# Optimization experiments

Measured on AMD Instinct MI355X. Metric: run time of the kernel, lower is better.

The kernel has to match this reference:

```python
import jax, jax.numpy as jnp
import numpy as np

N, E = 50000, 640000
D_IN, D_HID, D_OUT, HEADS = 128, 128, 128, 2


def _lin_init(k, fan_in, fan_out):
    return jax.random.normal(k, (fan_in, fan_out), jnp.float32) / np.sqrt(fan_in)


def setup_inputs() -> dict:
    key = jax.random.key(0)
    ks = jax.random.split(key, 20)
    inp = {
        "x": jax.random.normal(ks[0], (N, D_IN), jnp.float32),
        "edge_index": jax.random.randint(ks[1], (2, E), 0, N, dtype=jnp.int32),
    }
    # layer 1: in -> hid (heads*per_head = 2 * 64 = 128)
    inp["Wq1"] = _lin_init(ks[2], D_IN, D_HID); inp["bq1"] = jnp.zeros((D_HID,), jnp.float32)
    inp["Wk1"] = _lin_init(ks[3], D_IN, D_HID); inp["bk1"] = jnp.zeros((D_HID,), jnp.float32)
    inp["Wv1"] = _lin_init(ks[4], D_IN, D_HID); inp["bv1"] = jnp.zeros((D_HID,), jnp.float32)
    inp["Ws1"] = _lin_init(ks[5], D_IN, D_HID); inp["bs1"] = jnp.zeros((D_HID,), jnp.float32)
    # layer 2: hid -> out
    inp["Wq2"] = _lin_init(ks[6], D_HID, D_OUT); inp["bq2"] = jnp.zeros((D_OUT,), jnp.float32)
    inp["Wk2"] = _lin_init(ks[7], D_HID, D_OUT); inp["bk2"] = jnp.zeros((D_OUT,), jnp.float32)
    inp["Wv2"] = _lin_init(ks[8], D_HID, D_OUT); inp["bv2"] = jnp.zeros((D_OUT,), jnp.float32)
    inp["Ws2"] = _lin_init(ks[9], D_HID, D_OUT); inp["bs2"] = jnp.zeros((D_OUT,), jnp.float32)
    return inp


def _transformer_conv(x, src, dst, Wq, bq, Wk, bk, Wv, bv, Ws, bs, heads):
    """PyG TransformerConv (concat=True, root_weight=True, eval mode)."""
    n = x.shape[0]
    C = Wq.shape[1] // heads  # per-head channels
    q = (x @ Wq + bq).reshape(n, heads, C)
    k = (x @ Wk + bk).reshape(n, heads, C)
    v = (x @ Wv + bv).reshape(n, heads, C)
    qi = q[dst]              # [E, H, C] gather at destination
    kj = k[src]              # [E, H, C] gather at source
    vj = v[src]              # [E, H, C]
    alpha = jnp.sum(qi * kj, axis=-1) / np.sqrt(C)   # [E, H]
    # segment softmax over incoming edges of each destination node
    amax = jax.ops.segment_max(alpha, dst, num_segments=n)   # [N, H]
    ex = jnp.exp(alpha - amax[dst])                            # [E, H]
    denom = jax.ops.segment_sum(ex, dst, num_segments=n)      # [N, H]
    a = ex / denom[dst]                                        # [E, H]
    msg = vj * a[..., None]                                    # [E, H, C]
    out = jax.ops.segment_sum(msg, dst, num_segments=n).reshape(n, heads * C)
    return out + x @ Ws + bs  # root (skip) connection


def reference(x, edge_index, Wq1, bq1, Wk1, bk1, Wv1, bv1, Ws1, bs1,
              Wq2, bq2, Wk2, bk2, Wv2, bv2, Ws2, bs2):
    src, dst = edge_index[0], edge_index[1]
    h = _transformer_conv(x, src, dst, Wq1, bq1, Wk1, bk1, Wv1, bv1, Ws1, bs1, HEADS)
    h = jax.nn.relu(h)
    return _transformer_conv(h, src, dst, Wq2, bq2, Wk2, bk2, Wv2, bv2, Ws2, bs2, HEADS)
```

## Files before the change

kernel.cpp:

```cpp
#include <hip/hip_runtime.h>
#include <math.h>

#define D 128

typedef float  f32x4  __attribute__((ext_vector_type(4)));
typedef short  bf16x8 __attribute__((ext_vector_type(8)));

__device__ inline unsigned short bf16r(float f) {
    unsigned u = __float_as_uint(f);
    u = (u + 0x7fff + ((u >> 16) & 1)) >> 16;
    return (unsigned short)u;
}
__device__ inline unsigned bf16pair(float a, float b) {
    return (unsigned)bf16r(a) | ((unsigned)bf16r(b) << 16);
}
__device__ inline float bf16lo(unsigned w) { return __uint_as_float(w << 16); }
__device__ inline float bf16hi(unsigned w) { return __uint_as_float(w & 0xffff0000u); }

__device__ inline void unpack8(uint4 w, float* f) {
    f[0] = bf16lo(w.x); f[1] = bf16hi(w.x);
    f[2] = bf16lo(w.y); f[3] = bf16hi(w.y);
    f[4] = bf16lo(w.z); f[5] = bf16hi(w.z);
    f[6] = bf16lo(w.w); f[7] = bf16hi(w.w);
}

__global__ __launch_bounds__(256)
void prep(const float* __restrict__ X, unsigned* __restrict__ Xb, int npairs,
          const float* __restrict__ W0, const float* __restrict__ W1,
          const float* __restrict__ W2, const float* __restrict__ W3,
          const float* __restrict__ W4, const float* __restrict__ W5,
          const float* __restrict__ W6, const float* __restrict__ W7,
          unsigned short* __restrict__ Wt,
          int* __restrict__ cnt, int* __restrict__ bh, int* __restrict__ bcur, int n)
{
    const int nxb = (npairs + 255) >> 8;
    const int nz  = (n + 255) >> 8;
    const int b = blockIdx.x;
    if (b < nxb) {
        int i = b * 256 + threadIdx.x;
        if (i < npairs) {
            float2 v = *(const float2*)&X[2 * i];
            Xb[i] = bf16pair(v.x, v.y);
        }
    } else if (b < nxb + nz) {
        int i = (b - nxb) * 256 + threadIdx.x;
        if (i < n) cnt[i] = 0;
    } else if (b < nxb + nz + 8) {
        int wi = b - nxb - nz;
        const float* Ws[8] = {W0, W1, W2, W3, W4, W5, W6, W7};
        const float* W = Ws[wi];
        unsigned short* o = Wt + wi * 16384;
        for (int i = threadIdx.x; i < 16384; i += 256) {
            int k = i >> 7, c = i & 127;
            o[c * 128 + k] = bf16r(W[i]);
        }
    } else {
        if (threadIdx.x < 64) { bh[threadIdx.x] = 0; bcur[threadIdx.x] = 0; }
    }
}

__global__ __launch_bounds__(256)
void gemm_mfma(const unsigned short* __restrict__ Xb, int n,
               const unsigned short* __restrict__ Wtall,
               const float* __restrict__ bq, const float* __restrict__ bk,
               const float* __restrict__ bv, const float* __restrict__ bs,
               unsigned short* __restrict__ Qp, unsigned short* __restrict__ Kp,
               unsigned short* __restrict__ Vp, unsigned short* __restrict__ Sp)
{
    const int w = blockIdx.x;
    const int rowBase = blockIdx.y * 128;
    const unsigned short* W = Wtall + w * 16384;
    const float* bias = (w == 0) ? bq : (w == 1) ? bk : (w == 2) ? bv : bs;
    unsigned short* plane = (w == 0) ? Qp : (w == 1) ? Kp : (w == 2) ? Vp : Sp;

    __shared__ unsigned short Asm[128 * 136];

    const int tid  = threadIdx.x;
    const int wave = tid >> 6;
    const int lane = tid & 63;
    const int wr   = wave >> 1;
    const int wc   = wave & 1;
    const int q16  = lane >> 4;
    const int r16  = lane & 15;

    #pragma unroll
    for (int i = 0; i < 8; ++i) {
        int g = tid + 256 * i;
        int m = g >> 4, c = g & 15;
        int row = rowBase + m; if (row >= n) row = n - 1;
        uint4 da = *(const uint4*)(Xb + (size_t)row * 128 + c * 8);
        *(uint4*)&Asm[m * 136 + c * 8] = da;
    }

    const unsigned short* Wbase = W + (size_t)(wc * 64 + r16) * 128 + q16 * 8;
    bf16x8 bcur[4], bnxt[4];
    #pragma unroll
    for (int nj = 0; nj < 4; ++nj)
        bcur[nj] = *(const bf16x8*)(Wbase + nj * 16 * 128);

    __syncthreads();

    f32x4 acc[4][4];
    #pragma unroll
    for (int mi = 0; mi < 4; ++mi)
        #pragma unroll
        for (int nj = 0; nj < 4; ++nj) acc[mi][nj] = (f32x4)(0.f);

    #pragma unroll
    for (int kc = 0; kc < 4; ++kc) {
        if (kc < 3) {
            #pragma unroll
            for (int nj = 0; nj < 4; ++nj)
                bnxt[nj] = *(const bf16x8*)(Wbase + nj * 16 * 128 + (kc + 1) * 32);
        }
        bf16x8 a[4];
        #pragma unroll
        for (int mi = 0; mi < 4; ++mi)
            a[mi] = *(const bf16x8*)&Asm[(wr * 64 + mi * 16 + r16) * 136 + kc * 32 + q16 * 8];
        #pragma unroll
        for (int mi = 0; mi < 4; ++mi)
            #pragma unroll
            for (int nj = 0; nj < 4; ++nj)
                acc[mi][nj] = __builtin_amdgcn_mfma_f32_16x16x32_bf16(a[mi], bcur[nj], acc[mi][nj], 0, 0, 0);
        #pragma unroll
        for (int nj = 0; nj < 4; ++nj) bcur[nj] = bnxt[nj];
    }

    __syncthreads();
    #pragma unroll
    for (int nj = 0; nj < 4; ++nj) {
        const int col = wc * 64 + nj * 16 + r16;
        const float bias_c = bias[col];
        #pragma unroll
        for (int mi = 0; mi < 4; ++mi) {
            const int rbase = wr * 64 + mi * 16 + q16 * 4;
            #pragma unroll
            for (int r = 0; r < 4; ++r)
                Asm[(rbase + r) * 132 + col] = bf16r(acc[mi][nj][r] + bias_c);
        }
    }
    __syncthreads();
    #pragma unroll
    for (int i = 0; i < 8; ++i) {
        int g = tid + 256 * i;
        int m = g >> 4, c = g & 15;
        int row = rowBase + m;
        if (row < n) {
            uint4 d2 = *(const uint4*)&Asm[m * 132 + c * 8];
            *(uint4*)(plane + (size_t)row * 128 + c * 8) = d2;
        }
    }
}

__global__ void degree_hist(const int* __restrict__ dst, int e,
                            int* __restrict__ cnt, int* __restrict__ rank)
{
    int i = blockIdx.x * blockDim.x + threadIdx.x;
    if (i < e) rank[i] = atomicAdd(&cnt[dst[i]], 1);
}

__global__ __launch_bounds__(256)
void scan_hist(const int* __restrict__ cnt, int n, int* __restrict__ bsum, int* __restrict__ bh)
{
    __shared__ int sm[256];
    __shared__ int lh[64];
    if (threadIdx.x < 64) lh[threadIdx.x] = 0;
    int i = blockIdx.x * 256 + threadIdx.x;
    int v = (i < n) ? cnt[i] : 0;
    sm[threadIdx.x] = v;
    __syncthreads();
    if (i < n) atomicAdd(&lh[min(v, 63)], 1);
    #pragma unroll
    for (int off = 128; off > 0; off >>= 1) {
        if (threadIdx.x < off) sm[threadIdx.x] += sm[threadIdx.x + off];
        __syncthreads();
    }
    if (threadIdx.x == 0) bsum[blockIdx.x] = sm[0];
    if (threadIdx.x < 64 && lh[threadIdx.x] > 0)
        atomicAdd(&bh[threadIdx.x], lh[threadIdx.x]);
}

__global__ __launch_bounds__(256)
void scan2(int* __restrict__ bsum, int nb, const int* __restrict__ bh, int* __restrict__ boff)
{
    __shared__ int sm[256];
    int v = (threadIdx.x < nb) ? bsum[threadIdx.x] : 0;
    sm[threadIdx.x] = v;
    __syncthreads();
    int acc = v;
    for (int off = 1; off < 256; off <<= 1) {
        int t = (threadIdx.x >= off) ? sm[threadIdx.x - off] : 0;
        __syncthreads();
        acc += t;
        sm[threadIdx.x] = acc;
        __syncthreads();
    }
    if (threadIdx.x < nb) bsum[threadIdx.x] = acc - v;
    if (threadIdx.x == 0) {
        int run = 0;
        for (int b = 63; b >= 0; --b) { boff[b] = run; run += bh[b]; }
    }
}

__global__ __launch_bounds__(256)
void scan3_scatter(const int* __restrict__ cnt, const int* __restrict__ bsum,
                   int* __restrict__ row_ptr, int n, int e,
                   const int* __restrict__ boff, int* __restrict__ bcur,
                   int* __restrict__ perm)
{
    __shared__ int sm[256];
    __shared__ int lh[64];
    __shared__ int lbase[64];
    if (threadIdx.x < 64) lh[threadIdx.x] = 0;
    __syncthreads();
    int i = blockIdx.x * 256 + threadIdx.x;
    int v = (i < n) ? cnt[i] : 0;
    sm[threadIdx.x] = v;
    int b = 0, local = 0;
    if (i < n) {
        b = min(v, 63);
        local = atomicAdd(&lh[b], 1);
    }
    __syncthreads();
    int acc = v;
    for (int off = 1; off < 256; off <<= 1) {
        int t = (threadIdx.x >= off) ? sm[threadIdx.x - off] : 0;
        __syncthreads();
        acc += t;
        sm[threadIdx.x] = acc;
        __syncthreads();
    }
    if (i < n) row_ptr[i] = bsum[blockIdx.x] + acc - v;
    if (blockIdx.x == 0 && threadIdx.x == 0) row_ptr[n] = e;
    if (threadIdx.x < 64 && lh[threadIdx.x] > 0)
        lbase[threadIdx.x] = atomicAdd(&bcur[threadIdx.x], lh[threadIdx.x]);
    __syncthreads();
    if (i < n) perm[boff[b] + lbase[b] + local] = i;
}

__global__ void edge_scatter(const int* __restrict__ src, const int* __restrict__ dst, int e,
                             const int* __restrict__ row_ptr, const int* __restrict__ rank,
                             int* __restrict__ csr_src)
{
    int i = blockIdx.x * blockDim.x + threadIdx.x;
    if (i < e) {
        int d = dst[i];
        csr_src[row_ptr[d] + rank[i]] = src[i];
    }
}

__global__ __launch_bounds__(256)
void attn(const uint4* __restrict__ Qp, const uint4* __restrict__ Kp,
          const uint4* __restrict__ Vp, const uint4* __restrict__ Sp,
          const int* __restrict__ row_ptr, const int* __restrict__ csr_src,
          const int* __restrict__ perm,
          float* __restrict__ outf, uint4* __restrict__ outb,
          int n, int do_relu)
{
    const int wid  = (blockIdx.x * 256 + threadIdx.x) >> 6;
    const int lane = threadIdx.x & 63;
    const int nq   = lane >> 4;
    const int l16  = lane & 15;
    const int nidx = wid * 4 + nq;
    const int node = (nidx < n) ? perm[nidx] : -1;

    float q[8];
    int beg = 0, end = 0;
    if (node >= 0) {
        uint4 qw = Qp[(size_t)node * 16 + l16];
        unpack8(qw, q);
        beg = row_ptr[node];
        end = row_ptr[node + 1];
    }

    float m = -INFINITY, l = 0.f;
    float acc[8] = {0.f, 0.f, 0.f, 0.f, 0.f, 0.f, 0.f, 0.f};

    int i = beg;
    while (i + 4 <= end) {
        int s0 = csr_src[i], s1 = csr_src[i+1], s2 = csr_src[i+2], s3 = csr_src[i+3];
        uint4 kw0 = Kp[(size_t)s0 * 16 + l16];
        uint4 kw1 = Kp[(size_t)s1 * 16 + l16];
        uint4 kw2 = Kp[(size_t)s2 * 16 + l16];
        uint4 kw3 = Kp[(size_t)s3 * 16 + l16];
        uint4 vw0 = Vp[(size_t)s0 * 16 + l16];
        uint4 vw1 = Vp[(size_t)s1 * 16 + l16];
        uint4 vw2 = Vp[(size_t)s2 * 16 + l16];
        uint4 vw3 = Vp[(size_t)s3 * 16 + l16];

        float kf[8];
        unpack8(kw0, kf);
        float d0 = q[0]*kf[0]+q[1]*kf[1]+q[2]*kf[2]+q[3]*kf[3]+q[4]*kf[4]+q[5]*kf[5]+q[6]*kf[6]+q[7]*kf[7];
        unpack8(kw1, kf);
        float d1 = q[0]*kf[0]+q[1]*kf[1]+q[2]*kf[2]+q[3]*kf[3]+q[4]*kf[4]+q[5]*kf[5]+q[6]*kf[6]+q[7]*kf[7];
        unpack8(kw2, kf);
        float d2 = q[0]*kf[0]+q[1]*kf[1]+q[2]*kf[2]+q[3]*kf[3]+q[4]*kf[4]+q[5]*kf[5]+q[6]*kf[6]+q[7]*kf[7];
        unpack8(kw3, kf);
        float d3 = q[0]*kf[0]+q[1]*kf[1]+q[2]*kf[2]+q[3]*kf[3]+q[4]*kf[4]+q[5]*kf[5]+q[6]*kf[6]+q[7]*kf[7];

        d0 += __shfl_xor(d0, 4, 64); d1 += __shfl_xor(d1, 4, 64);
        d2 += __shfl_xor(d2, 4, 64); d3 += __shfl_xor(d3, 4, 64);
        d0 += __shfl_xor(d0, 2, 64); d1 += __shfl_xor(d1, 2, 64);
        d2 += __shfl_xor(d2, 2, 64); d3 += __shfl_xor(d3, 2, 64);
        d0 += __shfl_xor(d0, 1, 64); d1 += __shfl_xor(d1, 1, 64);
        d2 += __shfl_xor(d2, 1, 64); d3 += __shfl_xor(d3, 1, 64);

        float a0 = d0 * 0.125f, a1 = d1 * 0.125f, a2 = d2 * 0.125f, a3 = d3 * 0.125f;
        float m4 = fmaxf(fmaxf(a0, a1), fmaxf(a2, a3));
        float mn = fmaxf(m, m4);
        float corr = __expf(m - mn);
        float p0 = __expf(a0 - mn), p1 = __expf(a1 - mn);
        float p2 = __expf(a2 - mn), p3 = __expf(a3 - mn);
        l = l * corr + (p0 + p1 + p2 + p3);

        float v0f[8], v1f[8], v2f[8], v3f[8];
        unpack8(vw0, v0f); unpack8(vw1, v1f); unpack8(vw2, v2f); unpack8(vw3, v3f);
        #pragma unroll
        for (int c2 = 0; c2 < 8; ++c2) {
            float t = acc[c2] * corr;
            t += p0 * v0f[c2]; t += p1 * v1f[c2];
            t += p2 * v2f[c2]; t += p3 * v3f[c2];
            acc[c2] = t;
        }
        m = mn;
        i += 4;
    }
    while (i < end) {
        int s = csr_src[i];
        uint4 kw = Kp[(size_t)s * 16 + l16];
        uint4 vw = Vp[(size_t)s * 16 + l16];
        float kf[8], vf[8];
        unpack8(kw, kf); unpack8(vw, vf);
        float part = q[0]*kf[0]+q[1]*kf[1]+q[2]*kf[2]+q[3]*kf[3]+q[4]*kf[4]+q[5]*kf[5]+q[6]*kf[6]+q[7]*kf[7];
        part += __shfl_xor(part, 4, 64);
        part += __shfl_xor(part, 2, 64);
        part += __shfl_xor(part, 1, 64);
        float alpha = part * 0.125f;
        float mn = fmaxf(m, alpha);
        float corr = __expf(m - mn);
        float p = __expf(alpha - mn);
        l = l * corr + p;
        #pragma unroll
        for (int c2 = 0; c2 < 8; ++c2) acc[c2] = acc[c2] * corr + p * vf[c2];
        m = mn;
        ++i;
    }

    if (node >= 0) {
        float inv = (l > 0.f) ? (1.f / l) : 0.f;
        float sv[8];
        unpack8(Sp[(size_t)node * 16 + l16], sv);
        float r[8];
        #pragma unroll
        for (int c2 = 0; c2 < 8; ++c2) r[c2] = acc[c2] * inv + sv[c2];
        if (do_relu) {
            #pragma unroll
            for (int c2 = 0; c2 < 8; ++c2) r[c2] = fmaxf(r[c2], 0.f);
        }
        if (outb) {
            uint4 o;
            o.x = bf16pair(r[0], r[1]); o.y = bf16pair(r[2], r[3]);
            o.z = bf16pair(r[4], r[5]); o.w = bf16pair(r[6], r[7]);
            outb[(size_t)node * 16 + l16] = o;
        } else {
            *(float4*)&outf[(size_t)node * 128 + l16 * 8]     = make_float4(r[0], r[1], r[2], r[3]);
            *(float4*)&outf[(size_t)node * 128 + l16 * 8 + 4] = make_float4(r[4], r[5], r[6], r[7]);
        }
    }
}

extern "C" void kernel_launch(void* const* d_in, const int* in_sizes, int n_in,
                              void* d_out, int out_size, void* d_ws, size_t ws_size,
                              hipStream_t stream)
{
    const float* x    = (const float*)d_in[0];
    const int*   edge = (const int*)d_in[1];
    const int n = in_sizes[0] / D;
    const int e = in_sizes[1] / 2;
    const int* srcv = edge;
    const int* dstv = edge + e;

    const float* Wq1 = (const float*)d_in[2];  const float* bq1 = (const float*)d_in[3];
    const float* Wk1 = (const float*)d_in[4];  const float* bk1 = (const float*)d_in[5];
    const float* Wv1 = (const float*)d_in[6];  const float* bv1 = (const float*)d_in[7];
    const float* Ws1 = (const float*)d_in[8];  const float* bs1 = (const float*)d_in[9];
    const float* Wq2 = (const float*)d_in[10]; const float* bq2 = (const float*)d_in[11];
    const float* Wk2 = (const float*)d_in[12]; const float* bk2 = (const float*)d_in[13];
    const float* Wv2 = (const float*)d_in[14]; const float* bv2 = (const float*)d_in[15];
    const float* Ws2 = (const float*)d_in[16]; const float* bs2 = (const float*)d_in[17];

    char* wsb = (char*)d_ws;
    size_t off = 0;
    auto alloc = [&](size_t bytes) -> void* {
        void* p = wsb + off;
        off += (bytes + 255) & ~(size_t)255;
        return p;
    };
    unsigned short* Qp = (unsigned short*)alloc((size_t)n * D * sizeof(unsigned short));
    unsigned short* Kp = (unsigned short*)alloc((size_t)n * D * sizeof(unsigned short));
    unsigned short* Vp = (unsigned short*)alloc((size_t)n * D * sizeof(unsigned short));
    unsigned short* Sp = (unsigned short*)alloc((size_t)n * D * sizeof(unsigned short));
    unsigned short* Xb = (unsigned short*)alloc((size_t)n * D * sizeof(unsigned short));
    unsigned short* Hu = (unsigned short*)alloc((size_t)n * D * sizeof(unsigned short));
    unsigned short* Wt = (unsigned short*)alloc(8 * 16384 * sizeof(unsigned short));
    int* cnt     = (int*)alloc((size_t)n * sizeof(int));
    int* row_ptr = (int*)alloc((size_t)(n + 1) * sizeof(int));
    int* bsum    = (int*)alloc(1024 * sizeof(int));
    int* perm    = (int*)alloc((size_t)n * sizeof(int));
    int* bh      = (int*)alloc(64 * sizeof(int));
    int* bcur    = (int*)alloc(64 * sizeof(int));
    int* boff    = (int*)alloc(64 * sizeof(int));
    int* rank    = (int*)alloc((size_t)e * sizeof(int));
    int* csr_src = (int*)alloc((size_t)e * sizeof(int));
    (void)ws_size; (void)n_in; (void)out_size;

    const int nb  = (n + 255) / 256;
    const int npairs = n * 64;
    const int nprep  = (npairs + 255) / 256 + nb + 8 + 1;

    prep<<<nprep, 256, 0, stream>>>(x, (unsigned*)Xb, npairs,
        Wq1, Wk1, Wv1, Ws1, Wq2, Wk2, Wv2, Ws2, Wt, cnt, bh, bcur, n);

    degree_hist<<<(e + 255) / 256, 256, 0, stream>>>(dstv, e, cnt, rank);
    scan_hist<<<nb, 256, 0, stream>>>(cnt, n, bsum, bh);
    scan2<<<1, 256, 0, stream>>>(bsum, nb, bh, boff);
    scan3_scatter<<<nb, 256, 0, stream>>>(cnt, bsum, row_ptr, n, e, boff, bcur, perm);
    edge_scatter<<<(e + 255) / 256, 256, 0, stream>>>(srcv, dstv, e, row_ptr, rank, csr_src);

    const dim3 ggrid(4, (n + 127) / 128);
    const int ablocks = ((n + 3) / 4 + 3) / 4;

    gemm_mfma<<<ggrid, 256, 0, stream>>>(Xb, n, Wt, bq1, bk1, bv1, bs1, Qp, Kp, Vp, Sp);
    attn<<<ablocks, 256, 0, stream>>>((const uint4*)Qp, (const uint4*)Kp, (const uint4*)Vp,
                                      (const uint4*)Sp, row_ptr, csr_src, perm,
                                      nullptr, (uint4*)Hu, n, 1);

    gemm_mfma<<<ggrid, 256, 0, stream>>>(Hu, n, Wt + 4 * 16384, bq2, bk2, bv2, bs2, Qp, Kp, Vp, Sp);
    attn<<<ablocks, 256, 0, stream>>>((const uint4*)Qp, (const uint4*)Kp, (const uint4*)Vp,
                                      (const uint4*)Sp, row_ptr, csr_src, perm,
                                      (float*)d_out, nullptr, n, 0);
}
```

Measured before the change: 338.0 us.

## Interleave K and V rows and software-pipeline edge gathers in attention

The GEMM now writes K and V into one interleaved buffer, 256 bf16 per node, so each source node's K and V sit in one contiguous 512-byte row. The attention kernel gathers from this combined buffer and double-buffers the 4-edge batches: it loads the next batch's K/V before computing on the current one, to hide gather latency. The double buffering needs more registers for the extra uint4 sets, which may lower occupancy.

```diff
diff --git a/kernel.cpp b/kernel.cpp
--- a/kernel.cpp
+++ b/kernel.cpp
@@ -64,14 +64,18 @@
                const unsigned short* __restrict__ Wtall,
                const float* __restrict__ bq, const float* __restrict__ bk,
                const float* __restrict__ bv, const float* __restrict__ bs,
-               unsigned short* __restrict__ Qp, unsigned short* __restrict__ Kp,
-               unsigned short* __restrict__ Vp, unsigned short* __restrict__ Sp)
+               unsigned short* __restrict__ Qp, unsigned short* __restrict__ KVp,
+               unsigned short* __restrict__ Sp)
 {
     const int w = blockIdx.x;
     const int rowBase = blockIdx.y * 128;
     const unsigned short* W = Wtall + w * 16384;
     const float* bias = (w == 0) ? bq : (w == 1) ? bk : (w == 2) ? bv : bs;
-    unsigned short* plane = (w == 0) ? Qp : (w == 1) ? Kp : (w == 2) ? Vp : Sp;
+    unsigned short* base; int rstride, coff;
+    if (w == 0)      { base = Qp;  rstride = 128; coff = 0; }
+    else if (w == 1) { base = KVp; rstride = 256; coff = 0; }
+    else if (w == 2) { base = KVp; rstride = 256; coff = 128; }
+    else             { base = Sp;  rstride = 128; coff = 0; }
 
     __shared__ unsigned short Asm[128 * 136];
 
@@ -147,7 +151,7 @@
         int row = rowBase + m;
         if (row < n) {
             uint4 d2 = *(const uint4*)&Asm[m * 132 + c * 8];
-            *(uint4*)(plane + (size_t)row * 128 + c * 8) = d2;
+            *(uint4*)(base + (size_t)row * rstride + coff + c * 8) = d2;
         }
     }
 }
@@ -249,9 +253,59 @@
     }
 }
 
-__global__ __launch_bounds__(256)
-void attn(const uint4* __restrict__ Qp, const uint4* __restrict__ Kp,
-          const uint4* __restrict__ Vp, const uint4* __restrict__ Sp,
+__device__ inline void load4(const uint4* __restrict__ KV, const int* __restrict__ csr,
+                             int i, int l16, uint4* k, uint4* v)
+{
+    int s0 = csr[i], s1 = csr[i+1], s2 = csr[i+2], s3 = csr[i+3];
+    k[0] = KV[(size_t)s0 * 32 + l16];      v[0] = KV[(size_t)s0 * 32 + 16 + l16];
+    k[1] = KV[(size_t)s1 * 32 + l16];      v[1] = KV[(size_t)s1 * 32 + 16 + l16];
+    k[2] = KV[(size_t)s2 * 32 + l16];      v[2] = KV[(size_t)s2 * 32 + 16 + l16];
+    k[3] = KV[(size_t)s3 * 32 + l16];      v[3] = KV[(size_t)s3 * 32 + 16 + l16];
+}
+
+__device__ inline void consume4(const uint4* k, const uint4* v, const float* q,
+                                float& m, float& l, float* acc)
+{
+    float kf[8];
+    unpack8(k[0], kf);
+    float d0 = q[0]*kf[0]+q[1]*kf[1]+q[2]*kf[2]+q[3]*kf[3]+q[4]*kf[4]+q[5]*kf[5]+q[6]*kf[6]+q[7]*kf[7];
+    unpack8(k[1], kf);
+    float d1 = q[0]*kf[0]+q[1]*kf[1]+q[2]*kf[2]+q[3]*kf[3]+q[4]*kf[4]+q[5]*kf[5]+q[6]*kf[6]+q[7]*kf[7];
+    unpack8(k[2], kf);
+    float d2 = q[0]*kf[0]+q[1]*kf[1]+q[2]*kf[2]+q[3]*kf[3]+q[4]*kf[4]+q[5]*kf[5]+q[6]*kf[6]+q[7]*kf[7];
+    unpack8(k[3], kf);
+    float d3 = q[0]*kf[0]+q[1]*kf[1]+q[2]*kf[2]+q[3]*kf[3]+q[4]*kf[4]+q[5]*kf[5]+q[6]*kf[6]+q[7]*kf[7];
+
+    d0 += __shfl_xor(d0, 4, 64); d1 += __shfl_xor(d1, 4, 64);
+    d2 += __shfl_xor(d2, 4, 64); d3 += __shfl_xor(d3, 4, 64);
+    d0 += __shfl_xor(d0, 2, 64); d1 += __shfl_xor(d1, 2, 64);
+    d2 += __shfl_xor(d2, 2, 64); d3 += __shfl_xor(d3, 2, 64);
+    d0 += __shfl_xor(d0, 1, 64); d1 += __shfl_xor(d1, 1, 64);
+    d2 += __shfl_xor(d2, 1, 64); d3 += __shfl_xor(d3, 1, 64);
+
+    float a0 = d0 * 0.125f, a1 = d1 * 0.125f, a2 = d2 * 0.125f, a3 = d3 * 0.125f;
+    float m4 = fmaxf(fmaxf(a0, a1), fmaxf(a2, a3));
+    float mn = fmaxf(m, m4);
+    float corr = __expf(m - mn);
+    float p0 = __expf(a0 - mn), p1 = __expf(a1 - mn);
+    float p2 = __expf(a2 - mn), p3 = __expf(a3 - mn);
+    l = l * corr + (p0 + p1 + p2 + p3);
+
+    float v0f[8], v1f[8], v2f[8], v3f[8];
+    unpack8(v[0], v0f); unpack8(v[1], v1f); unpack8(v[2], v2f); unpack8(v[3], v3f);
+    #pragma unroll
+    for (int c2 = 0; c2 < 8; ++c2) {
+        float t = acc[c2] * corr;
+        t += p0 * v0f[c2]; t += p1 * v1f[c2];
+        t += p2 * v2f[c2]; t += p3 * v3f[c2];
+        acc[c2] = t;
+    }
+    m = mn;
+}
+
+__global__ __launch_bounds__(256)
+void attn(const uint4* __restrict__ Qp, const uint4* __restrict__ KV,
+          const uint4* __restrict__ Sp,
           const int* __restrict__ row_ptr, const int* __restrict__ csr_src,
           const int* __restrict__ perm,
           float* __restrict__ outf, uint4* __restrict__ outb,
@@ -277,58 +331,29 @@
     float acc[8] = {0.f, 0.f, 0.f, 0.f, 0.f, 0.f, 0.f, 0.f};
 
     int i = beg;
-    while (i + 4 <= end) {
-        int s0 = csr_src[i], s1 = csr_src[i+1], s2 = csr_src[i+2], s3 = csr_src[i+3];
-        uint4 kw0 = Kp[(size_t)s0 * 16 + l16];
-        uint4 kw1 = Kp[(size_t)s1 * 16 + l16];
-        uint4 kw2 = Kp[(size_t)s2 * 16 + l16];
-        uint4 kw3 = Kp[(size_t)s3 * 16 + l16];
-        uint4 vw0 = Vp[(size_t)s0 * 16 + l16];
-        uint4 vw1 = Vp[(size_t)s1 * 16 + l16];
-        uint4 vw2 = Vp[(size_t)s2 * 16 + l16];
-        uint4 vw3 = Vp[(size_t)s3 * 16 + l16];
-
-        float kf[8];
-        unpack8(kw0, kf);
-        float d0 = q[0]*kf[0]+q[1]*kf[1]+q[2]*kf[2]+q[3]*kf[3]+q[4]*kf[4]+q[5]*kf[5]+q[6]*kf[6]+q[7]*kf[7];
-        unpack8(kw1, kf);
-        float d1 = q[0]*kf[0]+q[1]*kf[1]+q[2]*kf[2]+q[3]*kf[3]+q[4]*kf[4]+q[5]*kf[5]+q[6]*kf[6]+q[7]*kf[7];
-        unpack8(kw2, kf);
-        float d2 = q[0]*kf[0]+q[1]*kf[1]+q[2]*kf[2]+q[3]*kf[3]+q[4]*kf[4]+q[5]*kf[5]+q[6]*kf[6]+q[7]*kf[7];
-        unpack8(kw3, kf);
-        float d3 = q[0]*kf[0]+q[1]*kf[1]+q[2]*kf[2]+q[3]*kf[3]+q[4]*kf[4]+q[5]*kf[5]+q[6]*kf[6]+q[7]*kf[7];
-
-        d0 += __shfl_xor(d0, 4, 64); d1 += __shfl_xor(d1, 4, 64);
-        d2 += __shfl_xor(d2, 4, 64); d3 += __shfl_xor(d3, 4, 64);
-        d0 += __shfl_xor(d0, 2, 64); d1 += __shfl_xor(d1, 2, 64);
-        d2 += __shfl_xor(d2, 2, 64); d3 += __shfl_xor(d3, 2, 64);
-        d0 += __shfl_xor(d0, 1, 64); d1 += __shfl_xor(d1, 1, 64);
-        d2 += __shfl_xor(d2, 1, 64); d3 += __shfl_xor(d3, 1, 64);
-
-        float a0 = d0 * 0.125f, a1 = d1 * 0.125f, a2 = d2 * 0.125f, a3 = d3 * 0.125f;
-        float m4 = fmaxf(fmaxf(a0, a1), fmaxf(a2, a3));
-        float mn = fmaxf(m, m4);
-        float corr = __expf(m - mn);
-        float p0 = __expf(a0 - mn), p1 = __expf(a1 - mn);
-        float p2 = __expf(a2 - mn), p3 = __expf(a3 - mn);
-        l = l * corr + (p0 + p1 + p2 + p3);
-
-        float v0f[8], v1f[8], v2f[8], v3f[8];
-        unpack8(vw0, v0f); unpack8(vw1, v1f); unpack8(vw2, v2f); unpack8(vw3, v3f);
-        #pragma unroll
-        for (int c2 = 0; c2 < 8; ++c2) {
-            float t = acc[c2] * corr;
-            t += p0 * v0f[c2]; t += p1 * v1f[c2];
-            t += p2 * v2f[c2]; t += p3 * v3f[c2];
-            acc[c2] = t;
-        }
-        m = mn;
+    uint4 ka[4], va[4], kb[4], vb[4];
+    if (i + 4 <= end) load4(KV, csr_src, i, l16, ka, va);
+    while (i + 8 <= end) {
+        load4(KV, csr_src, i + 4, l16, kb, vb);
+        consume4(ka, va, q, m, l, acc);
+        i += 4;
+        if (i + 8 <= end) {
+            load4(KV, csr_src, i + 4, l16, ka, va);
+            consume4(kb, vb, q, m, l, acc);
+            i += 4;
+        } else {
+            #pragma unroll
+            for (int t = 0; t < 4; ++t) { ka[t] = kb[t]; va[t] = vb[t]; }
+        }
+    }
+    if (i + 4 <= end) {
+        consume4(ka, va, q, m, l, acc);
         i += 4;
     }
     while (i < end) {
         int s = csr_src[i];
-        uint4 kw = Kp[(size_t)s * 16 + l16];
-        uint4 vw = Vp[(size_t)s * 16 + l16];
+        uint4 kw = KV[(size_t)s * 32 + l16];
+        uint4 vw = KV[(size_t)s * 32 + 16 + l16];
         float kf[8], vf[8];
         unpack8(kw, kf); unpack8(vw, vf);
         float part = q[0]*kf[0]+q[1]*kf[1]+q[2]*kf[2]+q[3]*kf[3]+q[4]*kf[4]+q[5]*kf[5]+q[6]*kf[6]+q[7]*kf[7];
@@ -396,13 +421,12 @@
         off += (bytes + 255) & ~(size_t)255;
         return p;
     };
-    unsigned short* Qp = (unsigned short*)alloc((size_t)n * D * sizeof(unsigned short));
-    unsigned short* Kp = (unsigned short*)alloc((size_t)n * D * sizeof(unsigned short));
-    unsigned short* Vp = (unsigned short*)alloc((size_t)n * D * sizeof(unsigned short));
-    unsigned short* Sp = (unsigned short*)alloc((size_t)n * D * sizeof(unsigned short));
-    unsigned short* Xb = (unsigned short*)alloc((size_t)n * D * sizeof(unsigned short));
-    unsigned short* Hu = (unsigned short*)alloc((size_t)n * D * sizeof(unsigned short));
-    unsigned short* Wt = (unsigned short*)alloc(8 * 16384 * sizeof(unsigned short));
+    unsigned short* Qp  = (unsigned short*)alloc((size_t)n * D * sizeof(unsigned short));
+    unsigned short* KVp = (unsigned short*)alloc((size_t)n * 2 * D * sizeof(unsigned short));
+    unsigned short* Sp  = (unsigned short*)alloc((size_t)n * D * sizeof(unsigned short));
+    unsigned short* Xb  = (unsigned short*)alloc((size_t)n * D * sizeof(unsigned short));
+    unsigned short* Hu  = (unsigned short*)alloc((size_t)n * D * sizeof(unsigned short));
+    unsigned short* Wt  = (unsigned short*)alloc(8 * 16384 * sizeof(unsigned short));
     int* cnt     = (int*)alloc((size_t)n * sizeof(int));
     int* row_ptr = (int*)alloc((size_t)(n + 1) * sizeof(int));
     int* bsum    = (int*)alloc(1024 * sizeof(int));
@@ -430,13 +454,11 @@
     const dim3 ggrid(4, (n + 127) / 128);
     const int ablocks = ((n + 3) / 4 + 3) / 4;
 
-    gemm_mfma<<<ggrid, 256, 0, stream>>>(Xb, n, Wt, bq1, bk1, bv1, bs1, Qp, Kp, Vp, Sp);
-    attn<<<ablocks, 256, 0, stream>>>((const uint4*)Qp, (const uint4*)Kp, (const uint4*)Vp,
-                                      (const uint4*)Sp, row_ptr, csr_src, perm,
-                                      nullptr, (uint4*)Hu, n, 1);
-
-    gemm_mfma<<<ggrid, 256, 0, stream>>>(Hu, n, Wt + 4 * 16384, bq2, bk2, bv2, bs2, Qp, Kp, Vp, Sp);
-    attn<<<ablocks, 256, 0, stream>>>((const uint4*)Qp, (const uint4*)Kp, (const uint4*)Vp,
-                                      (const uint4*)Sp, row_ptr, csr_src, perm,
-                                      (float*)d_out, nullptr, n, 0);
-}
+    gemm_mfma<<<ggrid, 256, 0, stream>>>(Xb, n, Wt, bq1, bk1, bv1, bs1, Qp, KVp, Sp);
+    attn<<<ablocks, 256, 0, stream>>>((const uint4*)Qp, (const uint4*)KVp, (const uint4*)Sp,
+                                      row_ptr, csr_src, perm, nullptr, (uint4*)Hu, n, 1);
+
+    gemm_mfma<<<ggrid, 256, 0, stream>>>(Hu, n, Wt + 4 * 16384, bq2, bk2, bv2, bs2, Qp, KVp, Sp);
+    attn<<<ablocks, 256, 0, stream>>>((const uint4*)Qp, (const uint4*)KVp, (const uint4*)Sp,
+                                      row_ptr, csr_src, perm, (float*)d_out, nullptr, n, 0);
+}
```

Result: no change. 335.1 us (-0.9%).

## Store keys in FP8, fuse edge scatter into GEMM, double-buffer attention gathers

Applied to the files above, without the earlier changes.

The GEMM now writes the K projection as FP8 (e4m3 via cvt_pk_fp8) rather than bf16, which halves the bytes gathered per edge for the attention dot product. The edge_scatter kernel is merged into the first GEMM launch as extra blocks, removing one launch and letting the two run concurrently. The attention loop is restructured to prefetch the next group of four neighbours' K/V while consuming the current group, and the skip-term load is hoisted to the start. FP8 keys lower attention-score precision, which may affect accuracy tolerance.

```diff
diff --git a/kernel.cpp b/kernel.cpp
--- a/kernel.cpp
+++ b/kernel.cpp
@@ -4,6 +4,7 @@
 #define D 128
 
 typedef float  f32x4  __attribute__((ext_vector_type(4)));
+typedef float  f32x2  __attribute__((ext_vector_type(2)));
 typedef short  bf16x8 __attribute__((ext_vector_type(8)));
 
 __device__ inline unsigned short bf16r(float f) {
@@ -22,6 +23,26 @@
     f[2] = bf16lo(w.y); f[3] = bf16hi(w.y);
     f[4] = bf16lo(w.z); f[5] = bf16hi(w.z);
     f[6] = bf16lo(w.w); f[7] = bf16hi(w.w);
+}
+
+__device__ inline unsigned pk_fp8x4(float a, float b, float c, float d) {
+    unsigned w = 0;
+    w = __builtin_amdgcn_cvt_pk_fp8_f32(a, b, w, false);
+    w = __builtin_amdgcn_cvt_pk_fp8_f32(c, d, w, true);
+    return w;
+}
+
+__device__ inline float dot8_fp8(const float* q, uint2 kw) {
+    f32x2 p;
+    p = __builtin_amdgcn_cvt_pk_f32_fp8((int)kw.x, false);
+    float s = q[0] * p.x + q[1] * p.y;
+    p = __builtin_amdgcn_cvt_pk_f32_fp8((int)kw.x, true);
+    s += q[2] * p.x + q[3] * p.y;
+    p = __builtin_amdgcn_cvt_pk_f32_fp8((int)kw.y, false);
+    s += q[4] * p.x + q[5] * p.y;
+    p = __builtin_amdgcn_cvt_pk_f32_fp8((int)kw.y, true);
+    s += q[6] * p.x + q[7] * p.y;
+    return s;
 }
 
 __global__ __launch_bounds__(256)
@@ -60,18 +81,30 @@
 }
 
 __global__ __launch_bounds__(256)
-void gemm_mfma(const unsigned short* __restrict__ Xb, int n,
-               const unsigned short* __restrict__ Wtall,
-               const float* __restrict__ bq, const float* __restrict__ bk,
-               const float* __restrict__ bv, const float* __restrict__ bs,
-               unsigned short* __restrict__ Qp, unsigned short* __restrict__ Kp,
-               unsigned short* __restrict__ Vp, unsigned short* __restrict__ Sp)
-{
-    const int w = blockIdx.x;
-    const int rowBase = blockIdx.y * 128;
+void gemm_es(const unsigned short* __restrict__ Xb, int n,
+             const unsigned short* __restrict__ Wtall,
+             const float* __restrict__ bq, const float* __restrict__ bk,
+             const float* __restrict__ bv, const float* __restrict__ bs,
+             unsigned short* __restrict__ Qp, unsigned char* __restrict__ K8,
+             unsigned short* __restrict__ Vp, unsigned short* __restrict__ Sp,
+             int gemmBlocks,
+             const int* __restrict__ src, const int* __restrict__ dst, int e,
+             const int* __restrict__ row_ptr, const int* __restrict__ rank,
+             int* __restrict__ csr_src)
+{
+    const int bid = blockIdx.x;
+    if (bid >= gemmBlocks) {
+        int i = (bid - gemmBlocks) * 256 + threadIdx.x;
+        if (i < e) {
+            int d = dst[i];
+            csr_src[row_ptr[d] + rank[i]] = src[i];
+        }
+        return;
+    }
+    const int w = bid & 3;
+    const int rowBase = (bid >> 2) * 128;
     const unsigned short* W = Wtall + w * 16384;
     const float* bias = (w == 0) ? bq : (w == 1) ? bk : (w == 2) ? bv : bs;
-    unsigned short* plane = (w == 0) ? Qp : (w == 1) ? Kp : (w == 2) ? Vp : Sp;
 
     __shared__ unsigned short Asm[128 * 136];
 
@@ -93,10 +126,10 @@
     }
 
     const unsigned short* Wbase = W + (size_t)(wc * 64 + r16) * 128 + q16 * 8;
-    bf16x8 bcur[4], bnxt[4];
+    bf16x8 bcu[4], bnx[4];
     #pragma unroll
     for (int nj = 0; nj < 4; ++nj)
-        bcur[nj] = *(const bf16x8*)(Wbase + nj * 16 * 128);
+        bcu[nj] = *(const bf16x8*)(Wbase + nj * 16 * 128);
 
     __syncthreads();
 
@@ -111,7 +144,7 @@
         if (kc < 3) {
             #pragma unroll
             for (int nj = 0; nj < 4; ++nj)
-                bnxt[nj] = *(const bf16x8*)(Wbase + nj * 16 * 128 + (kc + 1) * 32);
+                bnx[nj] = *(const bf16x8*)(Wbase + nj * 16 * 128 + (kc + 1) * 32);
         }
         bf16x8 a[4];
         #pragma unroll
@@ -121,9 +154,9 @@
         for (int mi = 0; mi < 4; ++mi)
             #pragma unroll
             for (int nj = 0; nj < 4; ++nj)
-                acc[mi][nj] = __builtin_amdgcn_mfma_f32_16x16x32_bf16(a[mi], bcur[nj], acc[mi][nj], 0, 0, 0);
-        #pragma unroll
-        for (int nj = 0; nj < 4; ++nj) bcur[nj] = bnxt[nj];
+                acc[mi][nj] = __builtin_amdgcn_mfma_f32_16x16x32_bf16(a[mi], bcu[nj], acc[mi][nj], 0, 0, 0);
+        #pragma unroll
+        for (int nj = 0; nj < 4; ++nj) bcu[nj] = bnx[nj];
     }
 
     __syncthreads();
@@ -140,14 +173,33 @@
         }
     }
     __syncthreads();
-    #pragma unroll
-    for (int i = 0; i < 8; ++i) {
-        int g = tid + 256 * i;
-        int m = g >> 4, c = g & 15;
-        int row = rowBase + m;
-        if (row < n) {
-            uint4 d2 = *(const uint4*)&Asm[m * 132 + c * 8];
-            *(uint4*)(plane + (size_t)row * 128 + c * 8) = d2;
+    if (w == 1) {
+        #pragma unroll
+        for (int i = 0; i < 8; ++i) {
+            int g = tid + 256 * i;
+            int m = g >> 4, c = g & 15;
+            int row = rowBase + m;
+            if (row < n) {
+                uint4 d2 = *(const uint4*)&Asm[m * 132 + c * 8];
+                float f[8];
+                unpack8(d2, f);
+                uint2 o;
+                o.x = pk_fp8x4(f[0], f[1], f[2], f[3]);
+                o.y = pk_fp8x4(f[4], f[5], f[6], f[7]);
+                *(uint2*)(K8 + (size_t)row * 128 + c * 8) = o;
+            }
+        }
+    } else {
+        unsigned short* plane = (w == 0) ? Qp : (w == 2) ? Vp : Sp;
+        #pragma unroll
+        for (int i = 0; i < 8; ++i) {
+            int g = tid + 256 * i;
+            int m = g >> 4, c = g & 15;
+            int row = rowBase + m;
+            if (row < n) {
+                uint4 d2 = *(const uint4*)&Asm[m * 132 + c * 8];
+                *(uint4*)(plane + (size_t)row * 128 + c * 8) = d2;
+            }
         }
     }
 }
@@ -238,19 +290,54 @@
     if (i < n) perm[boff[b] + lbase[b] + local] = i;
 }
 
-__global__ void edge_scatter(const int* __restrict__ src, const int* __restrict__ dst, int e,
-                             const int* __restrict__ row_ptr, const int* __restrict__ rank,
-                             int* __restrict__ csr_src)
-{
-    int i = blockIdx.x * blockDim.x + threadIdx.x;
-    if (i < e) {
-        int d = dst[i];
-        csr_src[row_ptr[d] + rank[i]] = src[i];
-    }
+__device__ inline void load4(const uint2* __restrict__ K8, const uint4* __restrict__ Vp,
+                             const int* __restrict__ csr, int i, int l16,
+                             uint2* k, uint4* v)
+{
+    int s0 = csr[i], s1 = csr[i+1], s2 = csr[i+2], s3 = csr[i+3];
+    k[0] = K8[(size_t)s0 * 16 + l16];  v[0] = Vp[(size_t)s0 * 16 + l16];
+    k[1] = K8[(size_t)s1 * 16 + l16];  v[1] = Vp[(size_t)s1 * 16 + l16];
+    k[2] = K8[(size_t)s2 * 16 + l16];  v[2] = Vp[(size_t)s2 * 16 + l16];
+    k[3] = K8[(size_t)s3 * 16 + l16];  v[3] = Vp[(size_t)s3 * 16 + l16];
+}
+
+__device__ inline void consume4(const uint2* k, const uint4* v, const float* q,
+                                float& m, float& l, float* acc)
+{
+    float d0 = dot8_fp8(q, k[0]);
+    float d1 = dot8_fp8(q, k[1]);
+    float d2 = dot8_fp8(q, k[2]);
+    float d3 = dot8_fp8(q, k[3]);
+
+    d0 += __shfl_xor(d0, 4, 64); d1 += __shfl_xor(d1, 4, 64);
+    d2 += __shfl_xor(d2, 4, 64); d3 += __shfl_xor(d3, 4, 64);
+    d0 += __shfl_xor(d0, 2, 64); d1 += __shfl_xor(d1, 2, 64);
+    d2 += __shfl_xor(d2, 2, 64); d3 += __shfl_xor(d3, 2, 64);
+    d0 += __shfl_xor(d0, 1, 64); d1 += __shfl_xor(d1, 1, 64);
+    d2 += __shfl_xor(d2, 1, 64); d3 += __shfl_xor(d3, 1, 64);
+
+    float a0 = d0 * 0.125f, a1 = d1 * 0.125f, a2 = d2 * 0.125f, a3 = d3 * 0.125f;
+    float m4 = fmaxf(fmaxf(a0, a1), fmaxf(a2, a3));
+    float mn = fmaxf(m, m4);
+    float corr = __expf(m - mn);
+    float p0 = __expf(a0 - mn), p1 = __expf(a1 - mn);
+    float p2 = __expf(a2 - mn), p3 = __expf(a3 - mn);
+    l = l * corr + (p0 + p1 + p2 + p3);
+
+    float v0f[8], v1f[8], v2f[8], v3f[8];
+    unpack8(v[0], v0f); unpack8(v[1], v1f); unpack8(v[2], v2f); unpack8(v[3], v3f);
+    #pragma unroll
+    for (int c2 = 0; c2 < 8; ++c2) {
+        float t = acc[c2] * corr;
+        t += p0 * v0f[c2]; t += p1 * v1f[c2];
+        t += p2 * v2f[c2]; t += p3 * v3f[c2];
+        acc[c2] = t;
+    }
+    m = mn;
 }
 
 __global__ __launch_bounds__(256)
-void attn(const uint4* __restrict__ Qp, const uint4* __restrict__ Kp,
+void attn(const uint4* __restrict__ Qp, const uint2* __restrict__ K8,
           const uint4* __restrict__ Vp, const uint4* __restrict__ Sp,
           const int* __restrict__ row_ptr, const int* __restrict__ csr_src,
           const int* __restrict__ perm,
@@ -265,10 +352,12 @@
     const int node = (nidx < n) ? perm[nidx] : -1;
 
     float q[8];
+    float sv[8];
     int beg = 0, end = 0;
     if (node >= 0) {
         uint4 qw = Qp[(size_t)node * 16 + l16];
         unpack8(qw, q);
+        unpack8(Sp[(size_t)node * 16 + l16], sv);
         beg = row_ptr[node];
         end = row_ptr[node + 1];
     }
@@ -277,61 +366,33 @@
     float acc[8] = {0.f, 0.f, 0.f, 0.f, 0.f, 0.f, 0.f, 0.f};
 
     int i = beg;
-    while (i + 4 <= end) {
-        int s0 = csr_src[i], s1 = csr_src[i+1], s2 = csr_src[i+2], s3 = csr_src[i+3];
-        uint4 kw0 = Kp[(size_t)s0 * 16 + l16];
-        uint4 kw1 = Kp[(size_t)s1 * 16 + l16];
-        uint4 kw2 = Kp[(size_t)s2 * 16 + l16];
-        uint4 kw3 = Kp[(size_t)s3 * 16 + l16];
-        uint4 vw0 = Vp[(size_t)s0 * 16 + l16];
-        uint4 vw1 = Vp[(size_t)s1 * 16 + l16];
-        uint4 vw2 = Vp[(size_t)s2 * 16 + l16];
-        uint4 vw3 = Vp[(size_t)s3 * 16 + l16];
-
-        float kf[8];
-        unpack8(kw0, kf);
-        float d0 = q[0]*kf[0]+q[1]*kf[1]+q[2]*kf[2]+q[3]*kf[3]+q[4]*kf[4]+q[5]*kf[5]+q[6]*kf[6]+q[7]*kf[7];
-        unpack8(kw1, kf);
-        float d1 = q[0]*kf[0]+q[1]*kf[1]+q[2]*kf[2]+q[3]*kf[3]+q[4]*kf[4]+q[5]*kf[5]+q[6]*kf[6]+q[7]*kf[7];
-        unpack8(kw2, kf);
-        float d2 = q[0]*kf[0]+q[1]*kf[1]+q[2]*kf[2]+q[3]*kf[3]+q[4]*kf[4]+q[5]*kf[5]+q[6]*kf[6]+q[7]*kf[7];
-        unpack8(kw3, kf);
-        float d3 = q[0]*kf[0]+q[1]*kf[1]+q[2]*kf[2]+q[3]*kf[3]+q[4]*kf[4]+q[5]*kf[5]+q[6]*kf[6]+q[7]*kf[7];
-
-        d0 += __shfl_xor(d0, 4, 64); d1 += __shfl_xor(d1, 4, 64);
-        d2 += __shfl_xor(d2, 4, 64); d3 += __shfl_xor(d3, 4, 64);
-        d0 += __shfl_xor(d0, 2, 64); d1 += __shfl_xor(d1, 2, 64);
-        d2 += __shfl_xor(d2, 2, 64); d3 += __shfl_xor(d3, 2, 64);
-        d0 += __shfl_xor(d0, 1, 64); d1 += __shfl_xor(d1, 1, 64);
-        d2 += __shfl_xor(d2, 1, 64); d3 += __shfl_xor(d3, 1, 64);
-
-        float a0 = d0 * 0.125f, a1 = d1 * 0.125f, a2 = d2 * 0.125f, a3 = d3 * 0.125f;
-        float m4 = fmaxf(fmaxf(a0, a1), fmaxf(a2, a3));
-        float mn = fmaxf(m, m4);
-        float corr = __expf(m - mn);
-        float p0 = __expf(a0 - mn), p1 = __expf(a1 - mn);
-        float p2 = __expf(a2 - mn), p3 = __expf(a3 - mn);
-        l = l * corr + (p0 + p1 + p2 + p3);
-
-        float v0f[8], v1f[8], v2f[8], v3f[8];
-        unpack8(vw0, v0f); unpack8(vw1, v1f); unpack8(vw2, v2f); unpack8(vw3, v3f);
-        #pragma unroll
-        for (int c2 = 0; c2 < 8; ++c2) {
-            float t = acc[c2] * corr;
-            t += p0 * v0f[c2]; t += p1 * v1f[c2];
-            t += p2 * v2f[c2]; t += p3 * v3f[c2];
-            acc[c2] = t;
-        }
-        m = mn;
+    uint2 ka[4], kb[4];
+    uint4 va[4], vb[4];
+    if (i + 4 <= end) load4(K8, Vp, csr_src, i, l16, ka, va);
+    while (i + 8 <= end) {
+        load4(K8, Vp, csr_src, i + 4, l16, kb, vb);
+        consume4(ka, va, q, m, l, acc);
+        i += 4;
+        if (i + 8 <= end) {
+            load4(K8, Vp, csr_src, i + 4, l16, ka, va);
+            consume4(kb, vb, q, m, l, acc);
+            i += 4;
+        } else {
+            #pragma unroll
+            for (int t = 0; t < 4; ++t) { ka[t] = kb[t]; va[t] = vb[t]; }
+        }
+    }
+    if (i + 4 <= end) {
+        consume4(ka, va, q, m, l, acc);
         i += 4;
     }
     while (i < end) {
         int s = csr_src[i];
-        uint4 kw = Kp[(size_t)s * 16 + l16];
+        uint2 kw = K8[(size_t)s * 16 + l16];
         uint4 vw = Vp[(size_t)s * 16 + l16];
-        float kf[8], vf[8];
-        unpack8(kw, kf); unpack8(vw, vf);
-        float part = q[0]*kf[0]+q[1]*kf[1]+q[2]*kf[2]+q[3]*kf[3]+q[4]*kf[4]+q[5]*kf[5]+q[6]*kf[6]+q[7]*kf[7];
+        float vf[8];
+        unpack8(vw, vf);
+        float part = dot8_fp8(q, kw);
         part += __shfl_xor(part, 4, 64);
         part += __shfl_xor(part, 2, 64);
         part += __shfl_xor(part, 1, 64);
@@ -348,8 +409,6 @@
 
     if (node >= 0) {
         float inv = (l > 0.f) ? (1.f / l) : 0.f;
-        float sv[8];
-        unpack8(Sp[(size_t)node * 16 + l16], sv);
         float r[8];
         #pragma unroll
         for (int c2 = 0; c2 < 8; ++c2) r[c2] = acc[c2] * inv + sv[c2];
@@ -397,7 +456,7 @@
         return p;
     };
     unsigned short* Qp = (unsigned short*)alloc((size_t)n * D * sizeof(unsigned short));
-    unsigned short* Kp = (unsigned short*)alloc((size_t)n * D * sizeof(unsigned short));
+    unsigned char*  K8 = (unsigned char*)alloc((size_t)n * D);
     unsigned short* Vp = (unsigned short*)alloc((size_t)n * D * sizeof(unsigned short));
     unsigned short* Sp = (unsigned short*)alloc((size_t)n * D * sizeof(unsigned short));
     unsigned short* Xb = (unsigned short*)alloc((size_t)n * D * sizeof(unsigned short));
@@ -425,18 +484,22 @@
     scan_hist<<<nb, 256, 0, stream>>>(cnt, n, bsum, bh);
     scan2<<<1, 256, 0, stream>>>(bsum, nb, bh, boff);
     scan3_scatter<<<nb, 256, 0, stream>>>(cnt, bsum, row_ptr, n, e, boff, bcur, perm);
-    edge_scatter<<<(e + 255) / 256, 256, 0, stream>>>(srcv, dstv, e, row_ptr, rank, csr_src);
-
-    const dim3 ggrid(4, (n + 127) / 128);
+
+    const int gemmBlocks = 4 * ((n + 127) / 128);
+    const int esBlocks   = (e + 255) / 256;
     const int ablocks = ((n + 3) / 4 + 3) / 4;
 
-    gemm_mfma<<<ggrid, 256, 0, stream>>>(Xb, n, Wt, bq1, bk1, bv1, bs1, Qp, Kp, Vp, Sp);
-    attn<<<ablocks, 256, 0, stream>>>((const uint4*)Qp, (const uint4*)Kp, (const uint4*)Vp,
+    gemm_es<<<gemmBlocks + esBlocks, 256, 0, stream>>>(Xb, n, Wt,
+        bq1, bk1, bv1, bs1, Qp, K8, Vp, Sp, gemmBlocks,
+        srcv, dstv, e, row_ptr, rank, csr_src);
+    attn<<<ablocks, 256, 0, stream>>>((const uint4*)Qp, (const uint2*)K8, (const uint4*)Vp,
                                       (const uint4*)Sp, row_ptr, csr_src, perm,
                                       nullptr, (uint4*)Hu, n, 1);
 
-    gemm_mfma<<<ggrid, 256, 0, stream>>>(Hu, n, Wt + 4 * 16384, bq2, bk2, bv2, bs2, Qp, Kp, Vp, Sp);
-    attn<<<ablocks, 256, 0, stream>>>((const uint4*)Qp, (const uint4*)Kp, (const uint4*)Vp,
+    gemm_es<<<gemmBlocks, 256, 0, stream>>>(Hu, n, Wt + 4 * 16384,
+        bq2, bk2, bv2, bs2, Qp, K8, Vp, Sp, gemmBlocks,
+        srcv, dstv, 0, row_ptr, rank, csr_src);
+    attn<<<ablocks, 256, 0, stream>>>((const uint4*)Qp, (const uint2*)K8, (const uint4*)Vp,
                                       (const uint4*)Sp, row_ptr, csr_src, perm,
                                       (float*)d_out, nullptr, n, 0);
 }
```

New measurement: 314.9 us. 1.07x faster.
